# Kernel tuning notes

Measured on AMD Instinct MI355X. Metric: run time of the kernel, lower is better.

## Reference

```python
import jax, jax.numpy as jnp
import numpy as np

D_MODEL = 1024
NUM_HEADS = 16
D_K = D_MODEL // NUM_HEADS


def setup_inputs() -> dict:
    key = jax.random.key(0)
    ks = jax.random.split(key, 11)
    B, T = 4, 2048
    s = 1.0 / np.sqrt(D_MODEL)
    return {
        'query': jax.random.normal(ks[0], (B, T, D_MODEL), jnp.float32),
        'key': jax.random.normal(ks[1], (B, T, D_MODEL), jnp.float32),
        'value': jax.random.normal(ks[2], (B, T, D_MODEL), jnp.float32),
        'Wq': jax.random.normal(ks[3], (D_MODEL, D_MODEL), jnp.float32) * s,
        'bq': jnp.zeros((D_MODEL,), jnp.float32),
        'Wk': jax.random.normal(ks[4], (D_MODEL, D_MODEL), jnp.float32) * s,
        'bk': jnp.zeros((D_MODEL,), jnp.float32),
        'Wv': jax.random.normal(ks[5], (D_MODEL, D_MODEL), jnp.float32) * s,
        'bv': jnp.zeros((D_MODEL,), jnp.float32),
        'Wo': jax.random.normal(ks[6], (D_MODEL, D_MODEL), jnp.float32) * s,
        'bo': jnp.zeros((D_MODEL,), jnp.float32),
    }


def reference(query, key, value, Wq, bq, Wk, bk, Wv, bv, Wo, bo):
    B, Tq, _ = query.shape
    Tk = key.shape[1]
    # projections (torch Linear: x @ W.T + b)
    q = (query @ Wq.T + bq).reshape(B, Tq, NUM_HEADS, D_K).transpose(0, 2, 1, 3)
    k = (key @ Wk.T + bk).reshape(B, Tk, NUM_HEADS, D_K).transpose(0, 2, 1, 3)
    v = (value @ Wv.T + bv).reshape(B, Tk, NUM_HEADS, D_K).transpose(0, 2, 1, 3)
    scale = 1.0 / jnp.sqrt(jnp.asarray(D_K, q.dtype))
    scores = jnp.einsum('bhqd,bhkd->bhqk', q, k) * scale  # [B,H,Tq,Tk]
    attn = jax.nn.softmax(scores, axis=-1)
    out = jnp.einsum('bhqk,bhkd->bhqd', attn, v)
    out = out.transpose(0, 2, 1, 3).reshape(B, Tq, D_MODEL)
    return out @ Wo.T + bo
```

## Files before the change

### kernel.cpp

```cpp
#include <hip/hip_runtime.h>

typedef unsigned short u16;
typedef unsigned int u32;
typedef __attribute__((ext_vector_type(8))) short bf16x8;
typedef __attribute__((ext_vector_type(4))) float f32x4;

__device__ inline u16 f2bf(float x) {
  union { float f; unsigned u; } v; v.f = x;
  unsigned r = v.u + 0x7fffu + ((v.u >> 16) & 1u);
  return (u16)(r >> 16);
}

__device__ inline u32 packbf2(float p0, float p1) {
  return __builtin_amdgcn_perm(__float_as_uint(p1), __float_as_uint(p0), 0x07060302u);
}

__device__ inline void gload16(const void* g, void* l) {
  __builtin_amdgcn_global_load_lds(
      (const __attribute__((address_space(1))) unsigned int*)g,
      (__attribute__((address_space(3))) unsigned int*)l,
      16, 0, 0);
}

__global__ void cvt_all(const float* __restrict__ q, const float* __restrict__ k,
                        const float* __restrict__ v,
                        const float* __restrict__ wq, const float* __restrict__ wk,
                        const float* __restrict__ wv, const float* __restrict__ wo,
                        u16* __restrict__ ws) {
  const size_t MT4 = (size_t)2 * 1024 * 1024;
  const int i = blockIdx.x * blockDim.x + threadIdx.x;
  const int t = blockIdx.y;
  float4 vv;
  ushort4 o;
  if (t < 3) {
    const float* src = (t == 0) ? q : (t == 1) ? k : v;
    vv = ((const float4*)src)[i];
    o.x = f2bf(vv.x); o.y = f2bf(vv.y); o.z = f2bf(vv.z); o.w = f2bf(vv.w);
    ((ushort4*)ws)[(size_t)t * MT4 + i] = o;
  } else {
    if (i >= (1 << 20)) return;
    const int w = i >> 18, j = i & 0x3FFFF;
    const float* src = (w == 0) ? wq : (w == 1) ? wk : (w == 2) ? wv : wo;
    vv = ((const float4*)src)[j];
    o.x = f2bf(vv.x); o.y = f2bf(vv.y); o.z = f2bf(vv.z); o.w = f2bf(vv.w);
    ((ushort4*)(ws + 3 * MT4 * 4))[i] = o;
  }
}

__global__ __launch_bounds__(256, 3) void gemm_qkv(
    const u16* __restrict__ Xq, const u16* __restrict__ Wqb,
    const float* __restrict__ bq_, const float* __restrict__ bk_,
    const float* __restrict__ bv_, u16* __restrict__ Qp)
{
  constexpr int N = 1024, K = 1024, BK = 32, NT = K / BK;
  constexpr size_t MT = (size_t)8192 * 1024, WT = (size_t)1024 * 1024;
  __shared__ __align__(16) u16 As[3][128 * BK];
  __shared__ __align__(16) u16 Bs[3][128 * BK];
  const int z = blockIdx.z;
  const u16* A = Xq + (size_t)z * MT;
  const u16* W = Wqb + (size_t)z * WT;
  const float* bias = (z == 0) ? bq_ : (z == 1) ? bk_ : bv_;
  u16* Cout = Qp + (size_t)z * MT;
  const bool vm = (z == 2);

  const int tid = threadIdx.x;
  const int wave = tid >> 6, lane = tid & 63;
  const int quad = lane >> 4, l16 = lane & 15;
  const int m0 = blockIdx.x * 128, n0 = blockIdx.y * 128;

  const int sA = wave * 2;
  const int srow = lane >> 2;
  const int skcol = ((lane & 3) ^ (srow & 3)) * 8;
  const int mloc = sA * 16 + srow;
  const int arow = vm ? ((mloc & 64) + (mloc & 3) * 16 + ((mloc & 63) >> 2)) : mloc;
  const int astep = vm ? 4 : 16;
  const u16* ag = A + (size_t)(m0 + arow) * K + skcol;
  const u16* bg = W + (size_t)(n0 + mloc) * K + skcol;

  const int wm = (wave >> 1) * 64, wn = (wave & 1) * 64;
  f32x4 acc[4][4] = {};

#define QKV_STAGE(s)                                   \
  do {                                                 \
    gload16(ag, As[s] + sA * 512);                     \
    gload16(ag + (size_t)astep * K, As[s] + sA * 512 + 512); \
    gload16(bg, Bs[s] + sA * 512);                     \
    gload16(bg + 16 * K, Bs[s] + sA * 512 + 512);      \
    ag += BK; bg += BK;                                \
  } while (0)

  QKV_STAGE(0);
  QKV_STAGE(1);

  int cb = 0, sb = 2;
  for (int kt = 0; kt < NT; ++kt) {
    if (kt + 1 < NT) asm volatile("s_waitcnt vmcnt(4)" ::: "memory");
    else             asm volatile("s_waitcnt vmcnt(0)" ::: "memory");
    __builtin_amdgcn_s_barrier();
    __builtin_amdgcn_sched_barrier(0);
    if (kt + 2 < NT) {
      QKV_STAGE(sb);
      sb = (sb == 2) ? 0 : sb + 1;
    }
    const u16* Ac = As[cb];
    const u16* Bc = Bs[cb];
    cb = (cb == 2) ? 0 : cb + 1;
    bf16x8 af[4], bf[4];
#pragma unroll
    for (int mi = 0; mi < 4; ++mi)
      af[mi] = *(const bf16x8*)(Ac + (wm + mi * 16 + l16) * BK + ((quad ^ (l16 & 3)) * 8));
#pragma unroll
    for (int ni = 0; ni < 4; ++ni)
      bf[ni] = *(const bf16x8*)(Bc + (wn + ni * 16 + l16) * BK + ((quad ^ (l16 & 3)) * 8));
#pragma unroll
    for (int mi = 0; mi < 4; ++mi)
#pragma unroll
      for (int ni = 0; ni < 4; ++ni)
        acc[mi][ni] = __builtin_amdgcn_mfma_f32_16x16x32_bf16(af[mi], bf[ni], acc[mi][ni], 0, 0, 0);
  }
#undef QKV_STAGE

#pragma unroll
  for (int ni = 0; ni < 4; ++ni) {
    const int col = n0 + wn + ni * 16 + l16;
    const float bv = bias[col];
#pragma unroll
    for (int mi = 0; mi < 4; ++mi) {
      const int mrow = m0 + wm + mi * 16 + quad * 4;
      f32x4 a = acc[mi][ni];
      if (!vm) {
#pragma unroll
        for (int r = 0; r < 4; ++r)
          Cout[(size_t)(mrow + r) * N + col] = f2bf(a[r] + bv);
      } else {
        const int bq = mrow >> 11, t = mrow & 2047;
        const int h = col >> 6, d = col & 63;
        ushort4 pk;
        pk.x = f2bf(a[0] + bv); pk.y = f2bf(a[1] + bv);
        pk.z = f2bf(a[2] + bv); pk.w = f2bf(a[3] + bv);
        *(ushort4*)(Cout + ((size_t)((bq * 16 + h) * 64 + d)) * 2048 + t) = pk;
      }
    }
  }
}

__global__ __launch_bounds__(256, 4) void gemm_wo(
    const u16* __restrict__ A, const u16* __restrict__ W,
    const float* __restrict__ bias, float* __restrict__ Cout)
{
  constexpr int N = 1024, K = 1024, BK = 32, NT = K / BK;
  __shared__ __align__(16) u16 As[3][128 * BK];
  __shared__ __align__(16) u16 Bs[3][64 * BK];
  const int tid = threadIdx.x;
  const int wave = tid >> 6, lane = tid & 63;
  const int quad = lane >> 4, l16 = lane & 15;
  const int m0 = blockIdx.x * 128, n0 = blockIdx.y * 64;

  const int sA = wave * 2;
  const int srow = lane >> 2;
  const int skcol = ((lane & 3) ^ (srow & 3)) * 8;
  const int mloc = sA * 16 + srow;
  const u16* ag = A + (size_t)(m0 + mloc) * K + skcol;
  const int brow = tid >> 2;
  const int bcol = ((tid & 3) ^ (brow & 3)) * 8;
  const u16* bg = W + (size_t)(n0 + brow) * K + bcol;

  const int wm = (wave >> 1) * 64, wn = (wave & 1) * 32;
  f32x4 acc[4][2] = {};

#define WO_STAGE(s)                                    \
  do {                                                 \
    gload16(ag, As[s] + sA * 512);                     \
    gload16(ag + 16 * K, As[s] + sA * 512 + 512);      \
    gload16(bg, Bs[s] + wave * 512);                   \
    ag += BK; bg += BK;                                \
  } while (0)

  WO_STAGE(0);
  WO_STAGE(1);

  int cb = 0, sb = 2;
  for (int kt = 0; kt < NT; ++kt) {
    if (kt + 1 < NT) asm volatile("s_waitcnt vmcnt(3)" ::: "memory");
    else             asm volatile("s_waitcnt vmcnt(0)" ::: "memory");
    __builtin_amdgcn_s_barrier();
    __builtin_amdgcn_sched_barrier(0);
    if (kt + 2 < NT) {
      WO_STAGE(sb);
      sb = (sb == 2) ? 0 : sb + 1;
    }
    const u16* Ac = As[cb];
    const u16* Bc = Bs[cb];
    cb = (cb == 2) ? 0 : cb + 1;
    bf16x8 af[4], bf[2];
#pragma unroll
    for (int mi = 0; mi < 4; ++mi)
      af[mi] = *(const bf16x8*)(Ac + (wm + mi * 16 + l16) * BK + ((quad ^ (l16 & 3)) * 8));
#pragma unroll
    for (int ni = 0; ni < 2; ++ni)
      bf[ni] = *(const bf16x8*)(Bc + (wn + ni * 16 + l16) * BK + ((quad ^ (l16 & 3)) * 8));
#pragma unroll
    for (int mi = 0; mi < 4; ++mi)
#pragma unroll
      for (int ni = 0; ni < 2; ++ni)
        acc[mi][ni] = __builtin_amdgcn_mfma_f32_16x16x32_bf16(af[mi], bf[ni], acc[mi][ni], 0, 0, 0);
  }
#undef WO_STAGE

#pragma unroll
  for (int ni = 0; ni < 2; ++ni) {
    const int col = n0 + wn + ni * 16 + l16;
    const float bv = bias[col];
#pragma unroll
    for (int mi = 0; mi < 4; ++mi) {
      const int mrow = m0 + wm + mi * 16 + quad * 4;
      f32x4 a = acc[mi][ni];
#pragma unroll
      for (int r = 0; r < 4; ++r)
        Cout[(size_t)(mrow + r) * N + col] = a[r] + bv;
    }
  }
}

__global__ __launch_bounds__(512, 4) void flash_attn(
    const u16* __restrict__ Qp, const u16* __restrict__ Kp,
    const u16* __restrict__ Vt, u16* __restrict__ Ctx)
{
  constexpr int TQ = 2048, DM = 1024, DK = 64;
  __shared__ __align__(16) u16 Ks[2][128 * 64];
  __shared__ __align__(16) u16 Vts[2][64 * 128];
  __shared__ __align__(16) u16 Ps[8][16 * 64];

  const int bh = blockIdx.x, b = bh >> 4, h = bh & 15;
  const int qt = blockIdx.y;
  const int tid = threadIdx.x, wave = tid >> 6, lane = tid & 63;
  const int quad = lane >> 4, l16 = lane & 15;
  const int q0 = qt * 256 + wave * 32;

  const int C0 = tid, C1 = 512 + tid;
  const int kr0 = C0 >> 3, kr1 = C1 >> 3;
  const u16* kp0 = Kp + (size_t)(b * TQ + kr0) * DM + h * DK + (((C0 & 7) ^ (kr0 & 7)) * 8);
  const u16* kp1 = Kp + (size_t)(b * TQ + kr1) * DM + h * DK + (((C1 & 7) ^ (kr1 & 7)) * 8);
  const int vd0 = C0 >> 4, vd1 = C1 >> 4;
  const u16* vp0 = Vt + (size_t)(bh * DK + vd0) * TQ + (((C0 & 15) ^ (vd0 & 15)) * 8);
  const u16* vp1 = Vt + (size_t)(bh * DK + vd1) * TQ + (((C1 & 15) ^ (vd1 & 15)) * 8);

  bf16x8 qf[2][2];
#pragma unroll
  for (int mi = 0; mi < 2; ++mi)
#pragma unroll
    for (int ks = 0; ks < 2; ++ks)
      qf[mi][ks] = *(const bf16x8*)(Qp + (size_t)(b * TQ + q0 + mi * 16 + l16) * DM
                                       + h * DK + ks * 32 + quad * 8);

  f32x4 O[2][4] = {};
  f32x4 lsum[2] = {};
  const float CS = 0.18033688011112042f;
  const float CB = 0.0028153f;

  bf16x8 onesv;
#pragma unroll
  for (int j = 0; j < 8; ++j) onesv[j] = (short)0x3F80;

  gload16(kp0, &Ks[0][C0 * 8]);
  gload16(kp1, &Ks[0][C1 * 8]);
  gload16(vp0, &Vts[0][C0 * 8]);
  gload16(vp1, &Vts[0][C1 * 8]);
  kp0 += 128 * DM; kp1 += 128 * DM; vp0 += 128; vp1 += 128;
  __syncthreads();

  const int kg = quad ^ (l16 & 7);
  int cur = 0;
  for (int kt = 0; kt < TQ / 128; ++kt) {
    if (kt + 1 < TQ / 128) {
      const int nb = cur ^ 1;
      gload16(kp0, &Ks[nb][C0 * 8]);
      gload16(kp1, &Ks[nb][C1 * 8]);
      gload16(vp0, &Vts[nb][C0 * 8]);
      gload16(vp1, &Vts[nb][C1 * 8]);
      kp0 += 128 * DM; kp1 += 128 * DM; vp0 += 128; vp1 += 128;
    }
    const u16* Kc = Ks[cur];
    const u16* Vc = Vts[cur];
    u16* Psw = Ps[wave];

#pragma unroll
    for (int g = 0; g < 2; ++g) {
      f32x4 Sg[2][4];
      __builtin_amdgcn_s_setprio(1);
#pragma unroll
      for (int cc = 0; cc < 4; ++cc) {
        const int row = (g * 4 + cc) * 16 + l16;
        bf16x8 kf0 = *(const bf16x8*)(Kc + row * 64 + kg * 8);
        bf16x8 kf1 = *(const bf16x8*)(Kc + row * 64 + (kg ^ 4) * 8);
#pragma unroll
        for (int mi = 0; mi < 2; ++mi) {
          f32x4 zz = {};
          zz = __builtin_amdgcn_mfma_f32_16x16x32_bf16(qf[mi][0], kf0, zz, 0, 0, 0);
          Sg[mi][cc] = __builtin_amdgcn_mfma_f32_16x16x32_bf16(qf[mi][1], kf1, zz, 0, 0, 0);
        }
      }
      __builtin_amdgcn_s_setprio(0);
      bf16x8 pf[2][2];
#pragma unroll
      for (int mi = 0; mi < 2; ++mi) {
#pragma unroll
        for (int r = 0; r < 4; ++r) {
          float e0 = __builtin_amdgcn_exp2f(fmaf(Sg[mi][0][r], CS, CB));
          float e1 = __builtin_amdgcn_exp2f(fmaf(Sg[mi][1][r], CS, CB));
          float e2 = __builtin_amdgcn_exp2f(fmaf(Sg[mi][2][r], CS, CB));
          float e3 = __builtin_amdgcn_exp2f(fmaf(Sg[mi][3][r], CS, CB));
          uint2 pk;
          pk.x = packbf2(e0, e1);
          pk.y = packbf2(e2, e3);
          const int pw = quad * 4 + r;
          *(uint2*)(&Psw[pw * 64 + ((l16 * 4) ^ ((pw & 7) << 3))]) = pk;
        }
#pragma unroll
        for (int ksl = 0; ksl < 2; ++ksl)
          pf[mi][ksl] = *(const bf16x8*)(&Psw[l16 * 64 + ((ksl * 32 + quad * 8) ^ ((l16 & 7) << 3))]);
#pragma unroll
        for (int ksl = 0; ksl < 2; ++ksl)
          lsum[mi] = __builtin_amdgcn_mfma_f32_16x16x32_bf16(pf[mi][ksl], onesv, lsum[mi], 0, 0, 0);
      }
      __builtin_amdgcn_s_setprio(1);
#pragma unroll
      for (int ksl = 0; ksl < 2; ++ksl)
#pragma unroll
        for (int ni = 0; ni < 4; ++ni) {
          const int gv = g * 8 + ksl * 4 + quad;
          bf16x8 vf = *(const bf16x8*)(Vc + (ni * 16 + l16) * 128 + ((gv ^ l16) * 8));
          O[0][ni] = __builtin_amdgcn_mfma_f32_16x16x32_bf16(pf[0][ksl], vf, O[0][ni], 0, 0, 0);
          O[1][ni] = __builtin_amdgcn_mfma_f32_16x16x32_bf16(pf[1][ksl], vf, O[1][ni], 0, 0, 0);
        }
      __builtin_amdgcn_s_setprio(0);
    }
    __syncthreads();
    cur ^= 1;
  }

#pragma unroll
  for (int mi = 0; mi < 2; ++mi)
#pragma unroll
    for (int r = 0; r < 4; ++r) {
      const float inv = 1.0f / lsum[mi][r];
      const int q = q0 + mi * 16 + quad * 4 + r;
#pragma unroll
      for (int ni = 0; ni < 4; ++ni) {
        const int col = h * DK + ni * 16 + l16;
        Ctx[(size_t)(b * TQ + q) * DM + col] = f2bf(O[mi][ni][r] * inv);
      }
    }
}

extern "C" void kernel_launch(void* const* d_in, const int* in_sizes, int n_in,
                              void* d_out, int out_size, void* d_ws, size_t ws_size,
                              hipStream_t stream)
{
  (void)in_sizes; (void)n_in; (void)out_size; (void)ws_size;
  const float* query = (const float*)d_in[0];
  const float* key_  = (const float*)d_in[1];
  const float* value = (const float*)d_in[2];
  const float* Wq = (const float*)d_in[3];
  const float* bq = (const float*)d_in[4];
  const float* Wk = (const float*)d_in[5];
  const float* bk = (const float*)d_in[6];
  const float* Wv = (const float*)d_in[7];
  const float* bv = (const float*)d_in[8];
  const float* Wo = (const float*)d_in[9];
  const float* bo = (const float*)d_in[10];

  const size_t MT = (size_t)4 * 2048 * 1024;
  const size_t WT = (size_t)1024 * 1024;
  u16* ws  = (u16*)d_ws;
  u16* Xq  = ws;
  u16* Wqb = Xq + 3 * MT;
  u16* Qp  = Wqb + 4 * WT;
  u16* Kp  = Qp + MT;
  u16* Vt  = Kp + MT;
  u16* Ctx = Vt + MT;
  u16* Wob = Wqb + 3 * WT;

  cvt_all<<<dim3(8192, 4), 256, 0, stream>>>(
      query, key_, value, Wq, Wk, Wv, Wo, ws);

  gemm_qkv<<<dim3(64, 8, 3), 256, 0, stream>>>(Xq, Wqb, bq, bk, bv, Qp);

  flash_attn<<<dim3(64, 8), 512, 0, stream>>>(Qp, Kp, Vt, Ctx);

  gemm_wo<<<dim3(64, 16), 256, 0, stream>>>(Ctx, Wob, bo, (float*)d_out);
}
```

Baseline: 331.2 us.

## Use 8-wave 512-thread blocks for QKV and output GEMMs with 128x128 tiles

Both projection GEMMs move from 4-wave to 8-wave blocks. Each wave now owns a 64x32 output sub-tile and issues one global-to-LDS load per operand per stage, with the vmcnt waits adjusted to match. The output-projection GEMM also grows its N tile from 64 to 128, which halves its grid and improves reuse of the A tile. The aim is more waves to hide latency and a lighter per-thread load, at the cost of a larger LDS footprint per block and fewer blocks in flight.

```diff
diff --git a/kernel.cpp b/kernel.cpp
--- a/kernel.cpp
+++ b/kernel.cpp
@@ -47,7 +47,7 @@
   }
 }
 
-__global__ __launch_bounds__(256, 3) void gemm_qkv(
+__global__ __launch_bounds__(512, 4) void gemm_qkv(
     const u16* __restrict__ Xq, const u16* __restrict__ Wqb,
     const float* __restrict__ bq_, const float* __restrict__ bk_,
     const float* __restrict__ bv_, u16* __restrict__ Qp)
@@ -68,24 +68,19 @@
   const int quad = lane >> 4, l16 = lane & 15;
   const int m0 = blockIdx.x * 128, n0 = blockIdx.y * 128;
 
-  const int sA = wave * 2;
-  const int srow = lane >> 2;
-  const int skcol = ((lane & 3) ^ (srow & 3)) * 8;
-  const int mloc = sA * 16 + srow;
-  const int arow = vm ? ((mloc & 64) + (mloc & 3) * 16 + ((mloc & 63) >> 2)) : mloc;
-  const int astep = vm ? 4 : 16;
-  const u16* ag = A + (size_t)(m0 + arow) * K + skcol;
-  const u16* bg = W + (size_t)(n0 + mloc) * K + skcol;
-
-  const int wm = (wave >> 1) * 64, wn = (wave & 1) * 64;
-  f32x4 acc[4][4] = {};
+  const int srow = tid >> 2;
+  const int sg = ((tid & 3) ^ (srow & 3)) * 8;
+  const int arowP = vm ? ((srow & 64) + (srow & 3) * 16 + ((srow & 63) >> 2)) : srow;
+  const u16* ag = A + (size_t)(m0 + arowP) * K + sg;
+  const u16* bg = W + (size_t)(n0 + srow) * K + sg;
+
+  const int wm = (wave >> 2) * 64, wn = (wave & 3) * 32;
+  f32x4 acc[4][2] = {};
 
 #define QKV_STAGE(s)                                   \
   do {                                                 \
-    gload16(ag, As[s] + sA * 512);                     \
-    gload16(ag + (size_t)astep * K, As[s] + sA * 512 + 512); \
-    gload16(bg, Bs[s] + sA * 512);                     \
-    gload16(bg + 16 * K, Bs[s] + sA * 512 + 512);      \
+    gload16(ag, As[s] + wave * 512);                   \
+    gload16(bg, Bs[s] + wave * 512);                   \
     ag += BK; bg += BK;                                \
   } while (0)
 
@@ -94,7 +89,7 @@
 
   int cb = 0, sb = 2;
   for (int kt = 0; kt < NT; ++kt) {
-    if (kt + 1 < NT) asm volatile("s_waitcnt vmcnt(4)" ::: "memory");
+    if (kt + 1 < NT) asm volatile("s_waitcnt vmcnt(2)" ::: "memory");
     else             asm volatile("s_waitcnt vmcnt(0)" ::: "memory");
     __builtin_amdgcn_s_barrier();
     __builtin_amdgcn_sched_barrier(0);
@@ -105,23 +100,23 @@
     const u16* Ac = As[cb];
     const u16* Bc = Bs[cb];
     cb = (cb == 2) ? 0 : cb + 1;
-    bf16x8 af[4], bf[4];
+    bf16x8 af[4], bf[2];
 #pragma unroll
     for (int mi = 0; mi < 4; ++mi)
       af[mi] = *(const bf16x8*)(Ac + (wm + mi * 16 + l16) * BK + ((quad ^ (l16 & 3)) * 8));
 #pragma unroll
-    for (int ni = 0; ni < 4; ++ni)
+    for (int ni = 0; ni < 2; ++ni)
       bf[ni] = *(const bf16x8*)(Bc + (wn + ni * 16 + l16) * BK + ((quad ^ (l16 & 3)) * 8));
 #pragma unroll
     for (int mi = 0; mi < 4; ++mi)
 #pragma unroll
-      for (int ni = 0; ni < 4; ++ni)
+      for (int ni = 0; ni < 2; ++ni)
         acc[mi][ni] = __builtin_amdgcn_mfma_f32_16x16x32_bf16(af[mi], bf[ni], acc[mi][ni], 0, 0, 0);
   }
 #undef QKV_STAGE
 
 #pragma unroll
-  for (int ni = 0; ni < 4; ++ni) {
+  for (int ni = 0; ni < 2; ++ni) {
     const int col = n0 + wn + ni * 16 + l16;
     const float bv = bias[col];
 #pragma unroll
@@ -144,34 +139,29 @@
   }
 }
 
-__global__ __launch_bounds__(256, 4) void gemm_wo(
+__global__ __launch_bounds__(512, 4) void gemm_wo(
     const u16* __restrict__ A, const u16* __restrict__ W,
     const float* __restrict__ bias, float* __restrict__ Cout)
 {
   constexpr int N = 1024, K = 1024, BK = 32, NT = K / BK;
   __shared__ __align__(16) u16 As[3][128 * BK];
-  __shared__ __align__(16) u16 Bs[3][64 * BK];
+  __shared__ __align__(16) u16 Bs[3][128 * BK];
   const int tid = threadIdx.x;
   const int wave = tid >> 6, lane = tid & 63;
   const int quad = lane >> 4, l16 = lane & 15;
-  const int m0 = blockIdx.x * 128, n0 = blockIdx.y * 64;
-
-  const int sA = wave * 2;
-  const int srow = lane >> 2;
-  const int skcol = ((lane & 3) ^ (srow & 3)) * 8;
-  const int mloc = sA * 16 + srow;
-  const u16* ag = A + (size_t)(m0 + mloc) * K + skcol;
-  const int brow = tid >> 2;
-  const int bcol = ((tid & 3) ^ (brow & 3)) * 8;
-  const u16* bg = W + (size_t)(n0 + brow) * K + bcol;
-
-  const int wm = (wave >> 1) * 64, wn = (wave & 1) * 32;
+  const int m0 = blockIdx.x * 128, n0 = blockIdx.y * 128;
+
+  const int srow = tid >> 2;
+  const int sg = ((tid & 3) ^ (srow & 3)) * 8;
+  const u16* ag = A + (size_t)(m0 + srow) * K + sg;
+  const u16* bg = W + (size_t)(n0 + srow) * K + sg;
+
+  const int wm = (wave >> 2) * 64, wn = (wave & 3) * 32;
   f32x4 acc[4][2] = {};
 
 #define WO_STAGE(s)                                    \
   do {                                                 \
-    gload16(ag, As[s] + sA * 512);                     \
-    gload16(ag + 16 * K, As[s] + sA * 512 + 512);      \
+    gload16(ag, As[s] + wave * 512);                   \
     gload16(bg, Bs[s] + wave * 512);                   \
     ag += BK; bg += BK;                                \
   } while (0)
@@ -181,7 +171,7 @@
 
   int cb = 0, sb = 2;
   for (int kt = 0; kt < NT; ++kt) {
-    if (kt + 1 < NT) asm volatile("s_waitcnt vmcnt(3)" ::: "memory");
+    if (kt + 1 < NT) asm volatile("s_waitcnt vmcnt(2)" ::: "memory");
     else             asm volatile("s_waitcnt vmcnt(0)" ::: "memory");
     __builtin_amdgcn_s_barrier();
     __builtin_amdgcn_sched_barrier(0);
@@ -384,9 +374,9 @@
   cvt_all<<<dim3(8192, 4), 256, 0, stream>>>(
       query, key_, value, Wq, Wk, Wv, Wo, ws);
 
-  gemm_qkv<<<dim3(64, 8, 3), 256, 0, stream>>>(Xq, Wqb, bq, bk, bv, Qp);
+  gemm_qkv<<<dim3(64, 8, 3), 512, 0, stream>>>(Xq, Wqb, bq, bk, bv, Qp);
 
   flash_attn<<<dim3(64, 8), 512, 0, stream>>>(Qp, Kp, Vt, Ctx);
 
-  gemm_wo<<<dim3(64, 16), 256, 0, stream>>>(Ctx, Wob, bo, (float*)d_out);
-}
+  gemm_wo<<<dim3(64, 8), 512, 0, stream>>>(Ctx, Wob, bo, (float*)d_out);
+}
```

After: 325.0 us. Within noise of the previous version (-1.9%).
